# Kernel tuning notes

Measured on AMD Instinct MI355X. Metric: run time of the kernel, lower is better.

Reference implementation:

```python
import jax, jax.numpy as jnp
import numpy as np

D_STATE = 16
D_CONV = 4
TOKEN = 8
GROUPS = 4
EPS = 1e-5


def _gn(x, w, b):
    # GroupNorm(GROUPS) over [B,C,H,W]
    B, C, H, W = x.shape
    xr = x.reshape(B, GROUPS, C // GROUPS, H * W)
    mu = xr.mean((2, 3), keepdims=True)
    var = xr.var((2, 3), keepdims=True)
    xn = ((xr - mu) * jax.lax.rsqrt(var + EPS)).reshape(B, C, H, W)
    return xn * w[None, :, None, None] + b[None, :, None, None]


def _mamba(x, in_w, conv_w, conv_b, xp_w, dt_w, dt_b, A_log, Dp, out_w, dt_rank):
    # mamba_ssm Mamba forward: x [B, L, d_model]
    Bn, L, _ = x.shape
    d_inner = conv_w.shape[0]
    xz = jnp.einsum('bld,ed->ble', x, in_w)          # [B,L,2*d_inner]
    xc, z = jnp.split(xz, 2, axis=-1)
    # causal depthwise conv1d (pad left d_conv-1)
    xt = jnp.pad(jnp.transpose(xc, (0, 2, 1)), ((0, 0), (0, 0), (D_CONV - 1, 0)))
    xt = jax.lax.conv_general_dilated(xt, conv_w[:, None, :], (1,), 'VALID',
                                      dimension_numbers=('NCH', 'OIH', 'NCH'),
                                      feature_group_count=d_inner)
    xc = jax.nn.silu(jnp.transpose(xt, (0, 2, 1)) + conv_b)
    dbl = jnp.einsum('ble,fe->blf', xc, xp_w)        # [B,L,dt_rank+2*d_state]
    dt = dbl[..., :dt_rank]
    Bm = dbl[..., dt_rank:dt_rank + D_STATE]
    Cm = dbl[..., dt_rank + D_STATE:]
    delta = jax.nn.softplus(jnp.einsum('blr,er->ble', dt, dt_w) + dt_b)
    A = -jnp.exp(A_log)                              # [d_inner, d_state]

    def step(h, inp):
        u_t, d_t, b_t, c_t = inp                     # [B,d_inner],[B,d_inner],[B,d_state],[B,d_state]
        dA = jnp.exp(d_t[..., None] * A)
        h = h * dA + (d_t * u_t)[..., None] * b_t[:, None, :]
        return h, jnp.sum(h * c_t[:, None, :], axis=-1)

    xs = (jnp.transpose(xc, (1, 0, 2)), jnp.transpose(delta, (1, 0, 2)),
          jnp.transpose(Bm, (1, 0, 2)), jnp.transpose(Cm, (1, 0, 2)))
    h0 = jnp.zeros((Bn, d_inner, D_STATE), x.dtype)
    _, ys = jax.lax.scan(step, h0, xs)
    y = (jnp.transpose(ys, (1, 0, 2)) + xc * Dp) * jax.nn.silu(z)
    return jnp.einsum('ble,de->bld', y, out_w)


def _mamba_params(key, d_model, dt_rank):
    d_inner = 2 * d_model
    ks = jax.random.split(key, 5)
    p = {}
    p['in_w'] = jax.random.normal(ks[0], (2 * d_inner, d_model)) / np.sqrt(d_model).astype(np.float32)
    p['conv_w'] = jax.random.normal(ks[1], (d_inner, D_CONV)) * 0.3
    p['conv_b'] = jnp.zeros((d_inner,))
    p['xp_w'] = jax.random.normal(ks[2], (dt_rank + 2 * D_STATE, d_inner)) / np.sqrt(d_inner).astype(np.float32)
    p['dt_w'] = jax.random.normal(ks[3], (d_inner, dt_rank)) / np.sqrt(dt_rank).astype(np.float32)
    p['dt_b'] = jnp.full((d_inner,), float(np.log(np.expm1(0.01))))
    p['A_log'] = jnp.log(jnp.broadcast_to(jnp.arange(1, D_STATE + 1, dtype=jnp.float32), (d_inner, D_STATE)))
    p['D'] = jnp.ones((d_inner,))
    p['out_w'] = jax.random.normal(ks[4], (d_model, d_inner)) / np.sqrt(d_inner).astype(np.float32)
    return p


def setup_inputs() -> dict:
    key = jax.random.key(0)
    k1, k2, k3 = jax.random.split(key, 3)
    B, C, H, W = 2, 64, 128, 128
    inp = {'x': jax.random.normal(k1, (B, C, H, W), dtype=jnp.float32)}
    spa = _mamba_params(k2, C, 4)
    spe = _mamba_params(k3, C // TOKEN, 1)
    for n, p in (('spa', spa), ('spe', spe)):
        for k, v in p.items():
            inp[f'{n}_{k}'] = v
    inp['spa_gn_w'] = jnp.ones((C,)); inp['spa_gn_b'] = jnp.zeros((C,))
    inp['spe_gn_w'] = jnp.ones((C,)); inp['spe_gn_b'] = jnp.zeros((C,))
    inp['fuse_w'] = jnp.full((2,), 0.5)
    return inp


def reference(x, spa_in_w, spa_conv_w, spa_conv_b, spa_xp_w, spa_dt_w, spa_dt_b,
              spa_A_log, spa_D, spa_out_w, spe_in_w, spe_conv_w, spe_conv_b,
              spe_xp_w, spe_dt_w, spe_dt_b, spe_A_log, spe_D, spe_out_w,
              spa_gn_w, spa_gn_b, spe_gn_w, spe_gn_b, fuse_w):
    B, C, H, W = x.shape
    # SpaMamba: scan over flattened spatial sequence
    xs = jnp.transpose(x, (0, 2, 3, 1)).reshape(B, H * W, C)
    ys = _mamba(xs, spa_in_w, spa_conv_w, spa_conv_b, spa_xp_w, spa_dt_w, spa_dt_b,
                spa_A_log, spa_D, spa_out_w, 4)
    spa = jnp.transpose(ys.reshape(B, H, W, C), (0, 3, 1, 2))
    spa = jax.nn.silu(_gn(spa, spa_gn_w, spa_gn_b)) + x
    # SpeMamba: scan over channel tokens per pixel (C == TOKEN * gc, no padding)
    gc = C // TOKEN
    xe = jnp.transpose(x, (0, 2, 3, 1)).reshape(B * H * W, TOKEN, gc)
    ye = _mamba(xe, spe_in_w, spe_conv_w, spe_conv_b, spe_xp_w, spe_dt_w, spe_dt_b,
                spe_A_log, spe_D, spe_out_w, 1)
    spe = jnp.transpose(ye.reshape(B, H, W, C), (0, 3, 1, 2))
    spe = jax.nn.silu(_gn(spe, spe_gn_w, spe_gn_b)) + x
    w = jax.nn.softmax(fuse_w)
    return spa * w[0] + spe * w[1] + x
```

## Files before the change

kernel.cpp:

```cpp
#include <hip/hip_runtime.h>
#include <math.h>


#define NB 2
#define NC 64
#define HW_ 16384
#define SCH 512
#define SLC 32

__device__ __forceinline__ float sigmoidf_(float v) { return 1.f / (1.f + __expf(-v)); }
__device__ __forceinline__ float siluf_(float v)    { return v * sigmoidf_(v); }
__device__ __forceinline__ float softplusf_(float v) {
    return v > 0.f ? v + log1pf(__expf(-v)) : log1pf(__expf(v));
}

#define K1_XS_OFF 8576
#define K1_XS_STR 68
#define K1_XCL_STR 132

__global__ __launch_bounds__(256) void k1_spatial_pre(
    const float* __restrict__ x, const float* __restrict__ in_w,
    const float* __restrict__ conv_w, const float* __restrict__ conv_b,
    const float* __restrict__ xp_w,
    float* __restrict__ xc_g, float* __restrict__ sz_g,
    float* __restrict__ dtp_g, float* __restrict__ Bm_g, float* __restrict__ Cm_g)
{
    __shared__ float smem[13132];
    const int tid = threadIdx.x;
    const int b   = blockIdx.x >> 8;
    const int l0  = (blockIdx.x & 255) << 6;

    for (int i = tid; i < 67 * 64; i += 256) {
        int c = i / 67;
        int tok = i - c * 67;
        int l = l0 + tok - 3;
        float v = (l >= 0) ? x[((size_t)b * NC + c) * HW_ + l] : 0.f;
        smem[K1_XS_OFF + tok * K1_XS_STR + c] = v;
    }
    __syncthreads();

    {
        const int e = tid & 127;
        const int half = tid >> 7;
        float w[64];
        #pragma unroll
        for (int q = 0; q < 16; ++q) {
            float4 wv = *(const float4*)(in_w + e * 64 + q * 4);
            w[q*4] = wv.x; w[q*4+1] = wv.y; w[q*4+2] = wv.z; w[q*4+3] = wv.w;
        }
        int t0 = half ? 34 : 0, t1 = half ? 67 : 34;
        for (int tok = t0; tok < t1; ++tok) {
            const float4* xr = (const float4*)(smem + K1_XS_OFF + tok * K1_XS_STR);
            float acc = 0.f;
            #pragma unroll
            for (int q = 0; q < 16; ++q) {
                float4 xv = xr[q];
                acc += w[q*4]*xv.x + w[q*4+1]*xv.y + w[q*4+2]*xv.z + w[q*4+3]*xv.w;
            }
            smem[tok * 128 + e] = acc;
        }
        #pragma unroll
        for (int q = 0; q < 16; ++q) {
            float4 wv = *(const float4*)(in_w + (128 + e) * 64 + q * 4);
            w[q*4] = wv.x; w[q*4+1] = wv.y; w[q*4+2] = wv.z; w[q*4+3] = wv.w;
        }
        int z0 = half * 32;
        for (int tok = z0; tok < z0 + 32; ++tok) {
            const float4* xr = (const float4*)(smem + K1_XS_OFF + (tok + 3) * K1_XS_STR);
            float acc = 0.f;
            #pragma unroll
            for (int q = 0; q < 16; ++q) {
                float4 xv = xr[q];
                acc += w[q*4]*xv.x + w[q*4+1]*xv.y + w[q*4+2]*xv.z + w[q*4+3]*xv.w;
            }
            sz_g[((size_t)(b * HW_ + l0 + tok)) * 128 + e] = siluf_(acc);
        }
    }
    __syncthreads();

    {
        const int e = tid & 127;
        float cw0 = conv_w[e*4], cw1 = conv_w[e*4+1], cw2 = conv_w[e*4+2], cw3 = conv_w[e*4+3];
        float cb = conv_b[e];
        float r[32];
        #pragma unroll
        for (int k = 0; k < 32; ++k) {
            int tok = (tid + k * 256) >> 7;
            float v = cb + cw0 * smem[(tok+0)*128 + e] + cw1 * smem[(tok+1)*128 + e]
                         + cw2 * smem[(tok+2)*128 + e] + cw3 * smem[(tok+3)*128 + e];
            v = siluf_(v);
            r[k] = v;
            xc_g[((size_t)(b * HW_ + l0 + tok)) * 128 + e] = v;
        }
        __syncthreads();
        #pragma unroll
        for (int k = 0; k < 32; ++k) {
            int tok = (tid + k * 256) >> 7;
            smem[tok * K1_XCL_STR + e] = r[k];
        }
    }
    __syncthreads();

    for (int i = tid; i < 64 * 32; i += 256) {
        int tok = i >> 5;
        int f = i & 31;
        const float4* xr = (const float4*)(smem + tok * K1_XCL_STR);
        const float4* wr = (const float4*)(xp_w + (4 + f) * 128);
        float acc = 0.f;
        #pragma unroll
        for (int q = 0; q < 32; ++q) {
            float4 a = xr[q], w4 = wr[q];
            acc += a.x*w4.x + a.y*w4.y + a.z*w4.z + a.w*w4.w;
        }
        size_t row = (size_t)(b * HW_ + l0 + tok);
        if (f < 16) Bm_g[row * 16 + f] = acc;
        else        Cm_g[row * 16 + (f - 16)] = acc;
    }
    {
        int tok = tid >> 2;
        int rr = tid & 3;
        const float4* xr = (const float4*)(smem + tok * K1_XCL_STR);
        const float4* wr = (const float4*)(xp_w + rr * 128);
        float acc = 0.f;
        #pragma unroll
        for (int q = 0; q < 32; ++q) {
            float4 a = xr[q], w4 = wr[q];
            acc += a.x*w4.x + a.y*w4.y + a.z*w4.z + a.w*w4.w;
        }
        dtp_g[(size_t)(b * HW_ + l0) * 4 + tid] = acc;
    }
}

__global__ __launch_bounds__(256) void k2_scan1(
    const float* __restrict__ xc_g, const float* __restrict__ Bm_g,
    const float* __restrict__ dtp_g, const float* __restrict__ dt_w,
    const float* __restrict__ dt_b, const float* __restrict__ A_log,
    float* __restrict__ cumA_g, float* __restrict__ hsum_g)
{
    __shared__ float su[SLC * 128];
    __shared__ float sB[SLC * 16];
    __shared__ float sdt[SLC * 4];
    const int tid = threadIdx.x;
    const int b = blockIdx.x >> 9;
    const int ch = blockIdx.x & 511;
    const size_t rowbase = (size_t)b * HW_ + ch * SLC;

    const float4* u4 = (const float4*)(xc_g + rowbase * 128);
    #pragma unroll
    for (int j = 0; j < 4; ++j) ((float4*)su)[tid + j * 256] = u4[tid + j * 256];
    if (tid < 128) ((float4*)sB)[tid] = ((const float4*)(Bm_g + rowbase * 16))[tid];
    if (tid < 32)  ((float4*)sdt)[tid] = ((const float4*)(dtp_g + rowbase * 4))[tid];

    const int e = tid >> 1;
    const int n0 = (tid & 1) * 8;
    float A[8];
    #pragma unroll
    for (int j = 0; j < 8; ++j) A[j] = -__expf(A_log[e * 16 + n0 + j]);
    float4 wdt = *(const float4*)(dt_w + e * 4);
    float dtb = dt_b[e];
    float h[8], cA[8];
    #pragma unroll
    for (int j = 0; j < 8; ++j) { h[j] = 0.f; cA[j] = 1.f; }
    __syncthreads();

    for (int t = 0; t < SLC; ++t) {
        float4 dv = *(const float4*)(sdt + t * 4);
        float d = softplusf_(wdt.x*dv.x + wdt.y*dv.y + wdt.z*dv.z + wdt.w*dv.w + dtb);
        float u = su[t * 128 + e];
        float4 b0 = *(const float4*)(sB + t * 16 + n0);
        float4 b1 = *(const float4*)(sB + t * 16 + n0 + 4);
        float Bv[8]; *(float4*)(Bv) = b0; *(float4*)(Bv + 4) = b1;
        float du = d * u;
        #pragma unroll
        for (int j = 0; j < 8; ++j) {
            float dA = __expf(d * A[j]);
            h[j] = h[j] * dA + du * Bv[j];
            cA[j] *= dA;
        }
    }
    size_t so = (size_t)blockIdx.x * 2048 + tid * 8;
    *(float4*)(cumA_g + so)     = *(float4*)(cA);
    *(float4*)(cumA_g + so + 4) = *(float4*)(cA + 4);
    *(float4*)(hsum_g + so)     = *(float4*)(h);
    *(float4*)(hsum_g + so + 4) = *(float4*)(h + 4);
}

__global__ __launch_bounds__(256) void k3_combine(
    const float* __restrict__ cumA_g, const float* __restrict__ hsum_g,
    float* __restrict__ Hin_g)
{
    int gid = blockIdx.x * 256 + threadIdx.x;
    int b = gid >> 11;
    int en = gid & 2047;
    float st = 0.f;
    size_t o = (size_t)b * SCH * 2048 + en;
    for (int cb = 0; cb < SCH; cb += 16) {
        float a[16], hs[16];
        #pragma unroll
        for (int k = 0; k < 16; ++k) {
            a[k]  = cumA_g[o + (size_t)k * 2048];
            hs[k] = hsum_g[o + (size_t)k * 2048];
        }
        #pragma unroll
        for (int k = 0; k < 16; ++k) {
            Hin_g[o + (size_t)k * 2048] = st;
            st = st * a[k] + hs[k];
        }
        o += (size_t)16 * 2048;
    }
}

__global__ __launch_bounds__(256) void k4_scan2(
    const float* __restrict__ xc_g, const float* __restrict__ sz_g,
    const float* __restrict__ Bm_g, const float* __restrict__ Cm_g,
    const float* __restrict__ dtp_g, const float* __restrict__ dt_w,
    const float* __restrict__ dt_b, const float* __restrict__ A_log,
    const float* __restrict__ Dp, const float* __restrict__ Hin_g,
    const float* __restrict__ out_w,
    float* __restrict__ spa_raw, float* __restrict__ part_spa)
{
    __shared__ float lds[9344];
    float* su  = lds;
    float* sB  = lds + 4096;
    float* sC  = lds + 4608;
    float* sdt = lds + 5120;
    float* yt  = lds + 5248;
    float* ot  = lds;
    __shared__ float wred[32];
    const int tid = threadIdx.x;
    const int b = blockIdx.x >> 9;
    const int ch = blockIdx.x & 511;
    const size_t rowbase = (size_t)b * HW_ + ch * SLC;

    const float4* u4 = (const float4*)(xc_g + rowbase * 128);
    #pragma unroll
    for (int j = 0; j < 4; ++j) ((float4*)su)[tid + j * 256] = u4[tid + j * 256];
    if (tid < 128) ((float4*)sB)[tid] = ((const float4*)(Bm_g + rowbase * 16))[tid];
    else           ((float4*)sC)[tid - 128] = ((const float4*)(Cm_g + rowbase * 16))[tid - 128];
    if (tid < 32)  ((float4*)sdt)[tid] = ((const float4*)(dtp_g + rowbase * 4))[tid];

    const int e = tid >> 1;
    const int nh = tid & 1;
    const int n0 = nh * 8;
    float A[8];
    #pragma unroll
    for (int j = 0; j < 8; ++j) A[j] = -__expf(A_log[e * 16 + n0 + j]);
    float4 wdt = *(const float4*)(dt_w + e * 4);
    float dtb = dt_b[e];
    float Dv = Dp[e];
    float h[8];
    size_t so = (size_t)blockIdx.x * 2048 + tid * 8;
    *(float4*)(h)     = *(const float4*)(Hin_g + so);
    *(float4*)(h + 4) = *(const float4*)(Hin_g + so + 4);
    __syncthreads();

    for (int t = 0; t < SLC; ++t) {
        float4 dv = *(const float4*)(sdt + t * 4);
        float d = softplusf_(wdt.x*dv.x + wdt.y*dv.y + wdt.z*dv.z + wdt.w*dv.w + dtb);
        float u = su[t * 128 + e];
        float4 b0 = *(const float4*)(sB + t * 16 + n0);
        float4 b1 = *(const float4*)(sB + t * 16 + n0 + 4);
        float4 c0 = *(const float4*)(sC + t * 16 + n0);
        float4 c1 = *(const float4*)(sC + t * 16 + n0 + 4);
        float Bv[8]; *(float4*)(Bv) = b0; *(float4*)(Bv + 4) = b1;
        float Cv[8]; *(float4*)(Cv) = c0; *(float4*)(Cv + 4) = c1;
        float du = d * u;
        float y = 0.f;
        #pragma unroll
        for (int j = 0; j < 8; ++j) {
            float dA = __expf(d * A[j]);
            h[j] = h[j] * dA + du * Bv[j];
            y += h[j] * Cv[j];
        }
        y += __shfl_xor(y, 1, 64);
        if (nh == 0) yt[t * 128 + e] = y + u * Dv;
    }
    __syncthreads();

    {
        const float4* sz4 = (const float4*)(sz_g + rowbase * 128);
        #pragma unroll
        for (int j = 0; j < 4; ++j) {
            int f = tid + j * 256;
            float4 yv = ((float4*)yt)[f];
            float4 sv = sz4[f];
            yv.x *= sv.x; yv.y *= sv.y; yv.z *= sv.z; yv.w *= sv.w;
            ((float4*)yt)[f] = yv;
        }
    }
    __syncthreads();

    for (int i = tid; i < 64 * SLC; i += 256) {
        int c = i & 63, t = i >> 6;
        const float4* wr = (const float4*)(out_w + c * 128);
        const float4* yr = (const float4*)(yt + t * 128);
        float acc = 0.f;
        #pragma unroll
        for (int q = 0; q < 32; ++q) {
            float4 w4 = wr[q], yv4 = yr[q];
            acc += w4.x*yv4.x + w4.y*yv4.y + w4.z*yv4.z + w4.w*yv4.w;
        }
        ot[c * 33 + t] = acc;
    }
    __syncthreads();

    for (int i = tid; i < 64 * SLC; i += 256) {
        int c = i >> 5, t = i & 31;
        spa_raw[((size_t)b * NC + c) * HW_ + ch * SLC + t] = ot[c * 33 + t];
    }
    float s[4], s2[4];
    #pragma unroll
    for (int g = 0; g < 4; ++g) {
        float a = 0.f, a2 = 0.f;
        for (int i = tid; i < 512; i += 256) {
            int c = 16 * g + (i >> 5), t = i & 31;
            float v = ot[c * 33 + t];
            a += v; a2 += v * v;
        }
        s[g] = a; s2[g] = a2;
    }
    #pragma unroll
    for (int g = 0; g < 4; ++g) {
        #pragma unroll
        for (int o = 1; o < 64; o <<= 1) {
            s[g]  += __shfl_xor(s[g], o, 64);
            s2[g] += __shfl_xor(s2[g], o, 64);
        }
    }
    if ((tid & 63) == 0) {
        int w = tid >> 6;
        #pragma unroll
        for (int g = 0; g < 4; ++g) { wred[w*8 + g*2] = s[g]; wred[w*8 + g*2 + 1] = s2[g]; }
    }
    __syncthreads();
    if (tid < 8)
        part_spa[blockIdx.x * 8 + tid] = wred[tid] + wred[8+tid] + wred[16+tid] + wred[24+tid];
}

__global__ __launch_bounds__(256, 2) void k5_spectral(
    const float* __restrict__ x, const float* __restrict__ in_w,
    const float* __restrict__ conv_w, const float* __restrict__ conv_b,
    const float* __restrict__ xp_w, const float* __restrict__ dt_w,
    const float* __restrict__ dt_b, const float* __restrict__ A_log,
    const float* __restrict__ Dp, const float* __restrict__ out_w,
    float* __restrict__ spe_raw, float* __restrict__ part_spe)
{
    __shared__ float xin[16 * 65];
    __shared__ float ys[16 * 136];
    __shared__ float outs[64 * 17];
    __shared__ float wred[32];
    const int tid = threadIdx.x;
    const int b = blockIdx.x >> 10;
    const int hw0 = (blockIdx.x & 1023) << 4;
    const int s = tid >> 4;
    const int l = tid & 15;
    const int base = tid & 48;

    for (int i = tid; i < 1024; i += 256) {
        int c = i >> 4, j = i & 15;
        xin[j * 65 + c] = x[((size_t)b * NC + c) * HW_ + hw0 + j];
    }

    float wdt[16];
    #pragma unroll
    for (int e = 0; e < 16; ++e) wdt[e] = xp_w[e];
    float wi0[8], wi1[8];
    #pragma unroll
    for (int c = 0; c < 8; ++c) { wi0[c] = in_w[l*8 + c]; wi1[c] = in_w[(l+16)*8 + c]; }
    float cw0 = conv_w[l*4], cw1 = conv_w[l*4+1], cw2 = conv_w[l*4+2], cw3 = conv_w[l*4+3];
    float cb = conv_b[l];
    float dtw = dt_w[l], dtb = dt_b[l];
    __syncthreads();

    float pre[8], sz[8];
    #pragma unroll
    for (int t = 0; t < 8; ++t) {
        float a0 = 0.f, a1 = 0.f;
        #pragma unroll
        for (int c = 0; c < 8; ++c) {
            float xv = xin[s * 65 + t * 8 + c];
            a0 += wi0[c] * xv; a1 += wi1[c] * xv;
        }
        pre[t] = a0; sz[t] = siluf_(a1);
    }
    float xcv[8];
    #pragma unroll
    for (int t = 0; t < 8; ++t) {
        float v = cb + cw3 * pre[t];
        if (t >= 1) v += cw2 * pre[t-1];
        if (t >= 2) v += cw1 * pre[t-2];
        if (t >= 3) v += cw0 * pre[t-3];
        xcv[t] = siluf_(v);
    }

    float wB[16], wC[16];
    #pragma unroll
    for (int e = 0; e < 16; ++e) {
        wB[e] = xp_w[(1 + l) * 16 + e];
        wC[e] = xp_w[(17 + l) * 16 + e];
    }
    float bn[8], cn[8], del[8];
    #pragma unroll
    for (int t = 0; t < 8; ++t) {
        float b_ = 0.f, c_ = 0.f, d0 = 0.f;
        #pragma unroll
        for (int e = 0; e < 16; ++e) {
            float xv = __shfl(xcv[t], base + e, 64);
            b_ += wB[e] * xv; c_ += wC[e] * xv; d0 += wdt[e] * xv;
        }
        bn[t] = b_; cn[t] = c_;
        del[t] = softplusf_(d0 * dtw + dtb);
    }

    float A[16];
    #pragma unroll
    for (int n = 0; n < 16; ++n) A[n] = -__expf(A_log[l * 16 + n]);
    float Dv = Dp[l];
    float h[16];
    #pragma unroll
    for (int n = 0; n < 16; ++n) h[n] = 0.f;
    #pragma unroll
    for (int t = 0; t < 8; ++t) {
        float d = del[t], u = xcv[t];
        float du = d * u;
        float y = 0.f;
        #pragma unroll
        for (int n = 0; n < 16; ++n) {
            float Bn = __shfl(bn[t], base + n, 64);
            float Cn = __shfl(cn[t], base + n, 64);
            float dA = __expf(d * A[n]);
            h[n] = h[n] * dA + du * Bn;
            y += h[n] * Cn;
        }
        ys[s * 136 + t * 17 + l] = (y + u * Dv) * sz[t];
    }
    __syncthreads();

    {
        int t = l >> 1;
        int db = (l & 1) * 4;
        #pragma unroll
        for (int jj = 0; jj < 4; ++jj) {
            int dd = db + jj;
            float acc = 0.f;
            #pragma unroll
            for (int e = 0; e < 16; ++e) acc += out_w[dd * 16 + e] * ys[s * 136 + t * 17 + e];
            outs[(t * 8 + dd) * 17 + s] = acc;
        }
    }
    __syncthreads();

    float sg[4], sg2[4];
    #pragma unroll
    for (int k = 0; k < 4; ++k) {
        int i = tid + k * 256;
        int c = i >> 4, j = i & 15;
        float v = outs[c * 17 + j];
        spe_raw[((size_t)b * NC + c) * HW_ + hw0 + j] = v;
        sg[k] = v; sg2[k] = v * v;
    }
    #pragma unroll
    for (int k = 0; k < 4; ++k) {
        #pragma unroll
        for (int o = 1; o < 64; o <<= 1) {
            sg[k]  += __shfl_xor(sg[k], o, 64);
            sg2[k] += __shfl_xor(sg2[k], o, 64);
        }
    }
    if ((tid & 63) == 0) {
        int w = tid >> 6;
        #pragma unroll
        for (int k = 0; k < 4; ++k) { wred[w*8 + k*2] = sg[k]; wred[w*8 + k*2 + 1] = sg2[k]; }
    }
    __syncthreads();
    if (tid < 8)
        part_spe[blockIdx.x * 8 + tid] = wred[tid] + wred[8+tid] + wred[16+tid] + wred[24+tid];
}

__global__ __launch_bounds__(256) void k5b_stats(
    const float* __restrict__ part_spa, const float* __restrict__ part_spe,
    float* __restrict__ stats)
{
    __shared__ float r1[256];
    __shared__ float fin[32];
    const int tid = threadIdx.x;
    const int combo = tid >> 4, sl = tid & 15;
    const int bb = combo >> 3, g = (combo >> 1) & 3, st = combo & 1;
    float acc = 0.f;
    for (int k = 0; k < 32; ++k)
        acc += part_spa[(bb * 512 + sl * 32 + k) * 8 + g * 2 + st];
    r1[tid] = acc;
    __syncthreads();
    if (tid < 16) { float a = 0.f; for (int k = 0; k < 16; ++k) a += r1[tid*16 + k]; fin[tid] = a; }
    __syncthreads();
    acc = 0.f;
    for (int k = 0; k < 64; ++k)
        acc += part_spe[(bb * 1024 + sl * 64 + k) * 8 + g * 2 + st];
    r1[tid] = acc;
    __syncthreads();
    if (tid < 16) { float a = 0.f; for (int k = 0; k < 16; ++k) a += r1[tid*16 + k]; fin[16 + tid] = a; }
    __syncthreads();
    if (tid < 16) {
        float S  = fin[(tid >> 3) * 16 + (tid & 7) * 2];
        float S2 = fin[(tid >> 3) * 16 + (tid & 7) * 2 + 1];
        const float N = 262144.f;
        float mu = S / N;
        float var = S2 / N - mu * mu;
        stats[tid * 2] = mu;
        stats[tid * 2 + 1] = rsqrtf(var + 1e-5f);
    }
}

__global__ __launch_bounds__(256) void k6_fuse(
    const float* __restrict__ x, const float* __restrict__ spa_raw,
    const float* __restrict__ spe_raw, const float* __restrict__ stats,
    const float* __restrict__ gwa, const float* __restrict__ gba,
    const float* __restrict__ gwe, const float* __restrict__ gbe,
    const float* __restrict__ fw, float* __restrict__ out)
{
    size_t i4 = (size_t)blockIdx.x * 256 + threadIdx.x;
    size_t base = i4 * 4;
    int b = (int)(base >> 20);
    int rem = (int)(base & 1048575);
    int c = rem >> 14;
    int g = c >> 4;
    int sidx = (b * 4 + g) * 2;
    float ma = stats[sidx],      ra = stats[sidx + 1];
    float me = stats[16 + sidx], re = stats[16 + sidx + 1];
    float wa = gwa[c], ba = gba[c], we = gwe[c], be = gbe[c];
    float f0 = fw[0], f1 = fw[1];
    float mx = fmaxf(f0, f1);
    float e0 = __expf(f0 - mx), e1 = __expf(f1 - mx);
    float inv = 1.f / (e0 + e1);
    float w0 = e0 * inv, w1 = e1 * inv;
    float4 xv = *(const float4*)(x + base);
    float4 av = *(const float4*)(spa_raw + base);
    float4 ev = *(const float4*)(spe_raw + base);
    float xr[4] = {xv.x, xv.y, xv.z, xv.w};
    float ar[4] = {av.x, av.y, av.z, av.w};
    float er[4] = {ev.x, ev.y, ev.z, ev.w};
    float orr[4];
    #pragma unroll
    for (int k = 0; k < 4; ++k) {
        float spa = siluf_((ar[k] - ma) * ra * wa + ba) + xr[k];
        float spe = siluf_((er[k] - me) * re * we + be) + xr[k];
        orr[k] = spa * w0 + spe * w1 + xr[k];
    }
    float4 ov = {orr[0], orr[1], orr[2], orr[3]};
    *(float4*)(out + base) = ov;
}

extern "C" void kernel_launch(void* const* d_in, const int* in_sizes, int n_in,
                              void* d_out, int out_size, void* d_ws, size_t ws_size,
                              hipStream_t stream)
{
    const float* x      = (const float*)d_in[0];
    const float* a_inw  = (const float*)d_in[1];
    const float* a_cw   = (const float*)d_in[2];
    const float* a_cb   = (const float*)d_in[3];
    const float* a_xp   = (const float*)d_in[4];
    const float* a_dtw  = (const float*)d_in[5];
    const float* a_dtb  = (const float*)d_in[6];
    const float* a_Alog = (const float*)d_in[7];
    const float* a_D    = (const float*)d_in[8];
    const float* a_ow   = (const float*)d_in[9];
    const float* e_inw  = (const float*)d_in[10];
    const float* e_cw   = (const float*)d_in[11];
    const float* e_cb   = (const float*)d_in[12];
    const float* e_xp   = (const float*)d_in[13];
    const float* e_dtw  = (const float*)d_in[14];
    const float* e_dtb  = (const float*)d_in[15];
    const float* e_Alog = (const float*)d_in[16];
    const float* e_D    = (const float*)d_in[17];
    const float* e_ow   = (const float*)d_in[18];
    const float* gwa    = (const float*)d_in[19];
    const float* gba    = (const float*)d_in[20];
    const float* gwe    = (const float*)d_in[21];
    const float* gbe    = (const float*)d_in[22];
    const float* fw     = (const float*)d_in[23];

    float* ws    = (float*)d_ws;
    float* xc    = ws;
    float* sz    = xc    + 4194304;
    float* Bm    = sz    + 4194304;
    float* Cm    = Bm    + 524288;
    float* dtp   = Cm    + 524288;
    float* cumA  = dtp   + 131072;
    float* hsum  = cumA  + 2097152;
    float* Hin   = hsum  + 2097152;
    float* spa_r = Hin   + 2097152;
    float* spe_r = spa_r + 2097152;
    float* pspa  = spe_r + 2097152;
    float* pspe  = pspa  + 8192;
    float* stats = pspe  + 16384;

    k1_spatial_pre<<<512, 256, 0, stream>>>(x, a_inw, a_cw, a_cb, a_xp,
                                            xc, sz, dtp, Bm, Cm);
    k2_scan1<<<1024, 256, 0, stream>>>(xc, Bm, dtp, a_dtw, a_dtb, a_Alog,
                                       cumA, hsum);
    k3_combine<<<16, 256, 0, stream>>>(cumA, hsum, Hin);
    k5_spectral<<<2048, 256, 0, stream>>>(x, e_inw, e_cw, e_cb, e_xp, e_dtw, e_dtb,
                                          e_Alog, e_D, e_ow, spe_r, pspe);
    k4_scan2<<<1024, 256, 0, stream>>>(xc, sz, Bm, Cm, dtp, a_dtw, a_dtb, a_Alog,
                                       a_D, Hin, a_ow, spa_r, pspa);
    k5b_stats<<<1, 256, 0, stream>>>(pspa, pspe, stats);
    k6_fuse<<<2048, 256, 0, stream>>>(x, spa_r, spe_r, stats, gwa, gba, gwe, gbe, fw,
                                      (float*)d_out);
}
```

Measured before the change: 413.4 us.

## Fuse chunk-local scan into spatial preprocessing kernel and restructure stats reductions

Folds the first-pass chunk scan (k2) into k1, so the per-chunk cumulative decay and partial state are computed from the xc, B and dt values already in shared memory instead of being reloaded from global memory in a separate launch. The spectral kernel now stages its B/C projection weights in shared memory, reorders the projection loop, and drops the 2-blocks-per-CU launch bound. Partial GroupNorm sums are written slot-major so the stats kernel can read them with coalesced float4 loads and reduce with shuffles. The trade-off is that k1 gets longer and holds more shared memory, and it has only 512 blocks doing the scan instead of k2's 1024, which reduces parallelism for that phase.

```diff
diff --git a/kernel.cpp b/kernel.cpp
--- a/kernel.cpp
+++ b/kernel.cpp
@@ -21,11 +21,15 @@
 __global__ __launch_bounds__(256) void k1_spatial_pre(
     const float* __restrict__ x, const float* __restrict__ in_w,
     const float* __restrict__ conv_w, const float* __restrict__ conv_b,
-    const float* __restrict__ xp_w,
+    const float* __restrict__ xp_w, const float* __restrict__ dt_w,
+    const float* __restrict__ dt_b, const float* __restrict__ A_log,
     float* __restrict__ xc_g, float* __restrict__ sz_g,
-    float* __restrict__ dtp_g, float* __restrict__ Bm_g, float* __restrict__ Cm_g)
+    float* __restrict__ dtp_g, float* __restrict__ Bm_g, float* __restrict__ Cm_g,
+    float* __restrict__ cumA_g, float* __restrict__ hsum_g)
 {
-    __shared__ float smem[13132];
+    __shared__ __align__(16) float smem[13132];
+    __shared__ __align__(16) float sB[64 * 16];
+    __shared__ __align__(16) float sdt[64 * 4];
     const int tid = threadIdx.x;
     const int b   = blockIdx.x >> 8;
     const int l0  = (blockIdx.x & 255) << 6;
@@ -113,14 +117,13 @@
             acc += a.x*w4.x + a.y*w4.y + a.z*w4.z + a.w*w4.w;
         }
         size_t row = (size_t)(b * HW_ + l0 + tok);
-        if (f < 16) Bm_g[row * 16 + f] = acc;
+        if (f < 16) { Bm_g[row * 16 + f] = acc; sB[tok * 16 + f] = acc; }
         else        Cm_g[row * 16 + (f - 16)] = acc;
     }
     {
         int tok = tid >> 2;
-        int rr = tid & 3;
         const float4* xr = (const float4*)(smem + tok * K1_XCL_STR);
-        const float4* wr = (const float4*)(xp_w + rr * 128);
+        const float4* wr = (const float4*)(xp_w + (tid & 3) * 128);
         float acc = 0.f;
         #pragma unroll
         for (int q = 0; q < 32; ++q) {
@@ -128,61 +131,46 @@
             acc += a.x*w4.x + a.y*w4.y + a.z*w4.z + a.w*w4.w;
         }
         dtp_g[(size_t)(b * HW_ + l0) * 4 + tid] = acc;
-    }
-}
-
-__global__ __launch_bounds__(256) void k2_scan1(
-    const float* __restrict__ xc_g, const float* __restrict__ Bm_g,
-    const float* __restrict__ dtp_g, const float* __restrict__ dt_w,
-    const float* __restrict__ dt_b, const float* __restrict__ A_log,
-    float* __restrict__ cumA_g, float* __restrict__ hsum_g)
-{
-    __shared__ float su[SLC * 128];
-    __shared__ float sB[SLC * 16];
-    __shared__ float sdt[SLC * 4];
-    const int tid = threadIdx.x;
-    const int b = blockIdx.x >> 9;
-    const int ch = blockIdx.x & 511;
-    const size_t rowbase = (size_t)b * HW_ + ch * SLC;
-
-    const float4* u4 = (const float4*)(xc_g + rowbase * 128);
-    #pragma unroll
-    for (int j = 0; j < 4; ++j) ((float4*)su)[tid + j * 256] = u4[tid + j * 256];
-    if (tid < 128) ((float4*)sB)[tid] = ((const float4*)(Bm_g + rowbase * 16))[tid];
-    if (tid < 32)  ((float4*)sdt)[tid] = ((const float4*)(dtp_g + rowbase * 4))[tid];
-
-    const int e = tid >> 1;
-    const int n0 = (tid & 1) * 8;
-    float A[8];
-    #pragma unroll
-    for (int j = 0; j < 8; ++j) A[j] = -__expf(A_log[e * 16 + n0 + j]);
-    float4 wdt = *(const float4*)(dt_w + e * 4);
-    float dtb = dt_b[e];
-    float h[8], cA[8];
-    #pragma unroll
-    for (int j = 0; j < 8; ++j) { h[j] = 0.f; cA[j] = 1.f; }
-    __syncthreads();
-
-    for (int t = 0; t < SLC; ++t) {
-        float4 dv = *(const float4*)(sdt + t * 4);
-        float d = softplusf_(wdt.x*dv.x + wdt.y*dv.y + wdt.z*dv.z + wdt.w*dv.w + dtb);
-        float u = su[t * 128 + e];
-        float4 b0 = *(const float4*)(sB + t * 16 + n0);
-        float4 b1 = *(const float4*)(sB + t * 16 + n0 + 4);
-        float Bv[8]; *(float4*)(Bv) = b0; *(float4*)(Bv + 4) = b1;
-        float du = d * u;
-        #pragma unroll
-        for (int j = 0; j < 8; ++j) {
-            float dA = __expf(d * A[j]);
-            h[j] = h[j] * dA + du * Bv[j];
-            cA[j] *= dA;
-        }
-    }
-    size_t so = (size_t)blockIdx.x * 2048 + tid * 8;
-    *(float4*)(cumA_g + so)     = *(float4*)(cA);
-    *(float4*)(cumA_g + so + 4) = *(float4*)(cA + 4);
-    *(float4*)(hsum_g + so)     = *(float4*)(h);
-    *(float4*)(hsum_g + so + 4) = *(float4*)(h + 4);
+        sdt[tid] = acc;
+    }
+    __syncthreads();
+
+    {
+        const int e = tid >> 1;
+        const int n0 = (tid & 1) * 8;
+        float A[8];
+        #pragma unroll
+        for (int j = 0; j < 8; ++j) A[j] = -__expf(A_log[e * 16 + n0 + j]);
+        float4 wdt = *(const float4*)(dt_w + e * 4);
+        float dtb = dt_b[e];
+        #pragma unroll 1
+        for (int cc = 0; cc < 2; ++cc) {
+            float h[8], cA[8];
+            #pragma unroll
+            for (int j = 0; j < 8; ++j) { h[j] = 0.f; cA[j] = 1.f; }
+            for (int t = cc * 32; t < cc * 32 + 32; ++t) {
+                float4 dv = *(const float4*)(sdt + t * 4);
+                float d = softplusf_(wdt.x*dv.x + wdt.y*dv.y + wdt.z*dv.z + wdt.w*dv.w + dtb);
+                float u = smem[t * K1_XCL_STR + e];
+                float4 b0 = *(const float4*)(sB + t * 16 + n0);
+                float4 b1 = *(const float4*)(sB + t * 16 + n0 + 4);
+                float Bv[8]; *(float4*)(Bv) = b0; *(float4*)(Bv + 4) = b1;
+                float du = d * u;
+                #pragma unroll
+                for (int j = 0; j < 8; ++j) {
+                    float dA = __expf(d * A[j]);
+                    h[j] = h[j] * dA + du * Bv[j];
+                    cA[j] *= dA;
+                }
+            }
+            int ch = ((blockIdx.x & 255) << 1) + cc;
+            size_t so = ((size_t)b * SCH + ch) * 2048 + tid * 8;
+            *(float4*)(cumA_g + so)     = *(float4*)(cA);
+            *(float4*)(cumA_g + so + 4) = *(float4*)(cA + 4);
+            *(float4*)(hsum_g + so)     = *(float4*)(h);
+            *(float4*)(hsum_g + so + 4) = *(float4*)(h + 4);
+        }
+    }
 }
 
 __global__ __launch_bounds__(256) void k3_combine(
@@ -219,7 +207,7 @@
     const float* __restrict__ out_w,
     float* __restrict__ spa_raw, float* __restrict__ part_spa)
 {
-    __shared__ float lds[9344];
+    __shared__ __align__(16) float lds[9344];
     float* su  = lds;
     float* sB  = lds + 4096;
     float* sC  = lds + 4608;
@@ -334,10 +322,10 @@
     }
     __syncthreads();
     if (tid < 8)
-        part_spa[blockIdx.x * 8 + tid] = wred[tid] + wred[8+tid] + wred[16+tid] + wred[24+tid];
-}
-
-__global__ __launch_bounds__(256, 2) void k5_spectral(
+        part_spa[tid * 1024 + blockIdx.x] = wred[tid] + wred[8+tid] + wred[16+tid] + wred[24+tid];
+}
+
+__global__ __launch_bounds__(256) void k5_spectral(
     const float* __restrict__ x, const float* __restrict__ in_w,
     const float* __restrict__ conv_w, const float* __restrict__ conv_b,
     const float* __restrict__ xp_w, const float* __restrict__ dt_w,
@@ -346,6 +334,8 @@
     float* __restrict__ spe_raw, float* __restrict__ part_spe)
 {
     __shared__ float xin[16 * 65];
+    __shared__ float sBw[16 * 17];
+    __shared__ float sCw[16 * 17];
     __shared__ float ys[16 * 136];
     __shared__ float outs[64 * 17];
     __shared__ float wred[32];
@@ -360,6 +350,11 @@
         int c = i >> 4, j = i & 15;
         xin[j * 65 + c] = x[((size_t)b * NC + c) * HW_ + hw0 + j];
     }
+    {
+        int l2 = tid >> 4, e2 = tid & 15;
+        sBw[l2 * 17 + e2] = xp_w[(1 + l2) * 16 + e2];
+        sCw[l2 * 17 + e2] = xp_w[(17 + l2) * 16 + e2];
+    }
 
     float wdt[16];
     #pragma unroll
@@ -393,24 +388,23 @@
         xcv[t] = siluf_(v);
     }
 
-    float wB[16], wC[16];
+    float bn[8], cn[8], dd0[8];
+    #pragma unroll
+    for (int t = 0; t < 8; ++t) { bn[t] = 0.f; cn[t] = 0.f; dd0[t] = 0.f; }
     #pragma unroll
     for (int e = 0; e < 16; ++e) {
-        wB[e] = xp_w[(1 + l) * 16 + e];
-        wC[e] = xp_w[(17 + l) * 16 + e];
-    }
-    float bn[8], cn[8], del[8];
-    #pragma unroll
-    for (int t = 0; t < 8; ++t) {
-        float b_ = 0.f, c_ = 0.f, d0 = 0.f;
-        #pragma unroll
-        for (int e = 0; e < 16; ++e) {
+        float wBe = sBw[l * 17 + e];
+        float wCe = sCw[l * 17 + e];
+        float wde = wdt[e];
+        #pragma unroll
+        for (int t = 0; t < 8; ++t) {
             float xv = __shfl(xcv[t], base + e, 64);
-            b_ += wB[e] * xv; c_ += wC[e] * xv; d0 += wdt[e] * xv;
-        }
-        bn[t] = b_; cn[t] = c_;
-        del[t] = softplusf_(d0 * dtw + dtb);
-    }
+            bn[t] += wBe * xv; cn[t] += wCe * xv; dd0[t] += wde * xv;
+        }
+    }
+    float del[8];
+    #pragma unroll
+    for (int t = 0; t < 8; ++t) del[t] = softplusf_(dd0[t] * dtw + dtb);
 
     float A[16];
     #pragma unroll
@@ -474,35 +468,48 @@
     }
     __syncthreads();
     if (tid < 8)
-        part_spe[blockIdx.x * 8 + tid] = wred[tid] + wred[8+tid] + wred[16+tid] + wred[24+tid];
+        part_spe[tid * 2048 + blockIdx.x] = wred[tid] + wred[8+tid] + wred[16+tid] + wred[24+tid];
 }
 
 __global__ __launch_bounds__(256) void k5b_stats(
     const float* __restrict__ part_spa, const float* __restrict__ part_spe,
     float* __restrict__ stats)
 {
-    __shared__ float r1[256];
-    __shared__ float fin[32];
+    __shared__ float fina[16], fine_[16];
     const int tid = threadIdx.x;
-    const int combo = tid >> 4, sl = tid & 15;
-    const int bb = combo >> 3, g = (combo >> 1) & 3, st = combo & 1;
-    float acc = 0.f;
-    for (int k = 0; k < 32; ++k)
-        acc += part_spa[(bb * 512 + sl * 32 + k) * 8 + g * 2 + st];
-    r1[tid] = acc;
-    __syncthreads();
-    if (tid < 16) { float a = 0.f; for (int k = 0; k < 16; ++k) a += r1[tid*16 + k]; fin[tid] = a; }
-    __syncthreads();
-    acc = 0.f;
-    for (int k = 0; k < 64; ++k)
-        acc += part_spe[(bb * 1024 + sl * 64 + k) * 8 + g * 2 + st];
-    r1[tid] = acc;
-    __syncthreads();
-    if (tid < 16) { float a = 0.f; for (int k = 0; k < 16; ++k) a += r1[tid*16 + k]; fin[16 + tid] = a; }
+    const int combo = tid >> 4;
+    const int ln = tid & 15;
+    const int slot = combo & 7, bb = combo >> 3;
+    {
+        const float4* p = (const float4*)(part_spa + slot * 1024 + bb * 512);
+        float a = 0.f;
+        #pragma unroll
+        for (int k = 0; k < 8; ++k) {
+            float4 v = p[ln * 8 + k];
+            a += v.x + v.y + v.z + v.w;
+        }
+        #pragma unroll
+        for (int o = 1; o < 16; o <<= 1) a += __shfl_xor(a, o, 64);
+        if (ln == 0) fina[combo] = a;
+    }
+    {
+        const float4* p = (const float4*)(part_spe + slot * 2048 + bb * 1024);
+        float a = 0.f;
+        #pragma unroll
+        for (int k = 0; k < 16; ++k) {
+            float4 v = p[ln * 16 + k];
+            a += v.x + v.y + v.z + v.w;
+        }
+        #pragma unroll
+        for (int o = 1; o < 16; o <<= 1) a += __shfl_xor(a, o, 64);
+        if (ln == 0) fine_[combo] = a;
+    }
     __syncthreads();
     if (tid < 16) {
-        float S  = fin[(tid >> 3) * 16 + (tid & 7) * 2];
-        float S2 = fin[(tid >> 3) * 16 + (tid & 7) * 2 + 1];
+        int branch = tid >> 3, bb2 = (tid >> 2) & 1, g = tid & 3;
+        const float* fin = branch ? fine_ : fina;
+        float S  = fin[bb2 * 8 + g * 2];
+        float S2 = fin[bb2 * 8 + g * 2 + 1];
         const float N = 262144.f;
         float mu = S / N;
         float var = S2 / N - mu * mu;
@@ -594,10 +601,9 @@
     float* pspe  = pspa  + 8192;
     float* stats = pspe  + 16384;
 
-    k1_spatial_pre<<<512, 256, 0, stream>>>(x, a_inw, a_cw, a_cb, a_xp,
-                                            xc, sz, dtp, Bm, Cm);
-    k2_scan1<<<1024, 256, 0, stream>>>(xc, Bm, dtp, a_dtw, a_dtb, a_Alog,
-                                       cumA, hsum);
+    k1_spatial_pre<<<512, 256, 0, stream>>>(x, a_inw, a_cw, a_cb, a_xp, a_dtw,
+                                            a_dtb, a_Alog,
+                                            xc, sz, dtp, Bm, Cm, cumA, hsum);
     k3_combine<<<16, 256, 0, stream>>>(cumA, hsum, Hin);
     k5_spectral<<<2048, 256, 0, stream>>>(x, e_inw, e_cw, e_cb, e_xp, e_dtw, e_dtb,
                                           e_Alog, e_D, e_ow, spe_r, pspe);
```

New measurement: 413.6 us. About the same (+0.1%).
